# Optimization experiments

Hardware: AMD Instinct MI355X
Metric: run time of the kernel (lower is better)

## Reference

```python
import jax, jax.numpy as jnp
import numpy as np

N, E, IN, H, C, L = 50000, 800000, 256, 128, 50, 3
EPS = 1e-5  # BatchNorm1d eps


def setup_inputs() -> dict:
    key = jax.random.key(0)
    ks = jax.random.split(key, 16)
    s = 0.05  # weight init scale
    return dict(
        features=jax.random.normal(ks[0], (N, IN), jnp.float32),
        src=jax.random.randint(ks[1], (E,), 0, N, jnp.int32),
        dst=jax.random.randint(ks[2], (E,), 0, N, jnp.int32),
        w_in=jax.random.normal(ks[3], (IN, H), jnp.float32) * s,
        b_in=jnp.zeros((H,), jnp.float32),
        gc_w=jax.random.normal(ks[4], (L, H, H), jnp.float32) * s,
        gc_b=jnp.zeros((L, H), jnp.float32),
        bn_gamma=jnp.ones((L, H), jnp.float32),
        bn_beta=jnp.zeros((L, H), jnp.float32),
        bn_mean=jax.random.normal(ks[5], (L, H), jnp.float32) * 0.1,
        bn_var=jax.random.uniform(ks[6], (L, H), jnp.float32, 0.5, 1.5),
        attn_w1=jax.random.normal(ks[7], (2 * H, H), jnp.float32) * s,
        attn_b1=jnp.zeros((H,), jnp.float32),
        attn_w2=jax.random.normal(ks[8], (H, 1), jnp.float32) * s,
        attn_b2=jnp.zeros((1,), jnp.float32),
        agg_w=jax.random.normal(ks[9], (2 * H, H), jnp.float32) * s,
        agg_b=jnp.zeros((H,), jnp.float32),
        out_w=jax.random.normal(ks[10], (H, C), jnp.float32) * s,
        out_b=jnp.zeros((C,), jnp.float32),
    )


def reference(features, src, dst, w_in, b_in, gc_w, gc_b, bn_gamma, bn_beta,
              bn_mean, bn_var, attn_w1, attn_b1, attn_w2, attn_b2,
              agg_w, agg_b, out_w, out_b):
    seg = lambda v, i: jax.ops.segment_sum(v, i, num_segments=N)
    ones_e = jnp.ones((E,), features.dtype)
    in_deg = seg(ones_e, dst)    # [N] in-degree (dst side)
    out_deg = seg(ones_e, src)   # [N] out-degree (src side)

    # input_encoder (dropout = identity at inference)
    h = jax.nn.relu(features @ w_in + b_in)  # [N, H]

    # aggregate_neighbor_types: copy_u + mean (0 for zero in-degree)
    neigh = seg(h[src], dst) / jnp.maximum(in_deg, 1.0)[:, None]
    agg = jax.nn.relu(jnp.concatenate([h, neigh], axis=1) @ agg_w + agg_b)

    # relation attention: MLP -> sigmoid gate, gated residual add
    a = jax.nn.relu(jnp.concatenate([h, agg], axis=1) @ attn_w1 + attn_b1)
    attn = jax.nn.sigmoid(a @ attn_w2 + attn_b2)  # [N, 1]
    h_att = h + agg * attn

    # DGL GraphConv norm='both', clamp(min=1), aggregate-then-matmul
    inv_out = jnp.maximum(out_deg, 1.0)[:, None] ** -0.5
    inv_in = jnp.maximum(in_deg, 1.0)[:, None] ** -0.5
    for i in range(L):
        x = h_att if i == 0 else h
        rst = seg((x * inv_out)[src], dst) * inv_in  # normalized SpMM
        rst = rst @ gc_w[i] + gc_b[i]
        # BatchNorm1d (eval: running stats)
        rst = (rst - bn_mean[i]) * (bn_gamma[i] * jax.lax.rsqrt(bn_var[i] + EPS)) + bn_beta[i]
        rst = jax.nn.relu(rst)
        if i > 0:
            rst = rst + h  # residual
        h = rst

    return h @ out_w + out_b  # [N, C]
```

## Files before the change

### kernel.cpp

```cpp
#include <hip/hip_runtime.h>
#include <hip/hip_fp16.h>
#include <math.h>

constexpr int NN  = 50000;
constexpr int EE  = 800000;
constexpr int INF_ = 256;
constexpr int HF  = 128;
constexpr int CC  = 50;
constexpr long NH = (long)NN * HF;
constexpr int NSL = 32;
constexpr int ESL = EE / NSL;
constexpr int CHK = 12500;
#define EPSV 1e-5f

enum { EPI_RELU = 0, EPI_NONE = 1, EPI_BN = 2, EPI_BN_RES = 3, EPI_ATTN = 4 };
enum { H16_NONE = 0, H16_SCALED = 2 };

typedef __attribute__((ext_vector_type(4))) float f32x4;
typedef __attribute__((ext_vector_type(8))) _Float16 f16x8;


__global__ __launch_bounds__(256) void count_partial2_kernel(
    const int4* __restrict__ dst4, const int4* __restrict__ src4,
    unsigned* __restrict__ pd, unsigned* __restrict__ ps) {
  __shared__ unsigned cnt[CHK];
  int bb = blockIdx.x;
  const int which = bb >> 7;
  bb &= 127;
  const int4* keys4 = which ? src4 : dst4;
  unsigned* partials = which ? ps : pd;
  const int chunk = bb & 3;
  const int sl = bb >> 2;
  for (int i = threadIdx.x; i < CHK; i += 256) cnt[i] = 0;
  __syncthreads();
  const int base4 = sl * (ESL / 4);
  const int lo = chunk * CHK;
  for (int i = threadIdx.x; i < ESL / 4; i += 256) {
    int4 k = keys4[base4 + i];
    int a;
    a = k.x - lo; if ((unsigned)a < (unsigned)CHK) atomicAdd(&cnt[a], 1u);
    a = k.y - lo; if ((unsigned)a < (unsigned)CHK) atomicAdd(&cnt[a], 1u);
    a = k.z - lo; if ((unsigned)a < (unsigned)CHK) atomicAdd(&cnt[a], 1u);
    a = k.w - lo; if ((unsigned)a < (unsigned)CHK) atomicAdd(&cnt[a], 1u);
  }
  __syncthreads();
  unsigned* p = partials + (long)sl * NN + lo;
  for (int i = threadIdx.x; i < CHK; i += 256) p[i] = cnt[i];
}

__global__ __launch_bounds__(256) void deg_scan_kernel(
    const unsigned* __restrict__ pd, const unsigned* __restrict__ ps,
    int* __restrict__ row_ptr, int* __restrict__ bsum,
    float* __restrict__ inv_mean, float* __restrict__ inv_in,
    float* __restrict__ inv_out) {
  __shared__ int sh[256];
  int n = blockIdx.x * 256 + threadIdx.x;
  unsigned di = 0, dz = 0;
  if (n < NN) {
    #pragma unroll 8
    for (int sl = 0; sl < NSL; ++sl) {
      di += pd[(long)sl * NN + n];
      dz += ps[(long)sl * NN + n];
    }
    float fdi = fmaxf((float)di, 1.f), fdz = fmaxf((float)dz, 1.f);
    inv_mean[n] = 1.f / fdi;
    inv_in[n]  = rsqrtf(fdi);
    inv_out[n] = rsqrtf(fdz);
  }
  int v = (n < NN) ? (int)di : 0;
  sh[threadIdx.x] = v;
  __syncthreads();
  #pragma unroll
  for (int off = 1; off < 256; off <<= 1) {
    int tv = (threadIdx.x >= off) ? sh[threadIdx.x - off] : 0;
    __syncthreads();
    sh[threadIdx.x] += tv;
    __syncthreads();
  }
  if (n < NN) row_ptr[n] = sh[threadIdx.x] - v;
  if (threadIdx.x == 255) bsum[blockIdx.x] = sh[255];
}

__global__ __launch_bounds__(256) void scan_block_kernel(const int* __restrict__ counts,
                                                         int* excl, int* bsum, int n) {
  __shared__ int sh[256];
  int i = blockIdx.x * 256 + threadIdx.x;
  int v = (i < n) ? counts[i] : 0;
  sh[threadIdx.x] = v;
  __syncthreads();
  #pragma unroll
  for (int off = 1; off < 256; off <<= 1) {
    int tv = (threadIdx.x >= off) ? sh[threadIdx.x - off] : 0;
    __syncthreads();
    sh[threadIdx.x] += tv;
    __syncthreads();
  }
  if (i < n) excl[i] = sh[threadIdx.x] - v;
  if (threadIdx.x == 255 && bsum) bsum[blockIdx.x] = sh[255];
}

__global__ void cursor_init_kernel(const int* __restrict__ row_ptr, const int* __restrict__ bsum,
                                   const unsigned* __restrict__ pd,
                                   unsigned* __restrict__ cur0,
                                   const float* __restrict__ inv_mean,
                                   const float* __restrict__ inv_in,
                                   int4* __restrict__ nodeinfo) {
  int n = blockIdx.x * 256 + threadIdx.x;
  if (n >= NN) return;
  unsigned start = (unsigned)(row_ptr[n] + bsum[n >> 8]);
  unsigned run = start;
  #pragma unroll 8
  for (int sl = 0; sl < NSL; ++sl) {
    cur0[(long)sl * NN + n] = run;
    run += pd[(long)sl * NN + n];
  }
  nodeinfo[n] = make_int4((int)start, (int)run,
                          __float_as_int(inv_mean[n]), __float_as_int(inv_in[n]));
}

__global__ __launch_bounds__(256) void fill_partial_kernel(
    const int4* __restrict__ dst4, const int4* __restrict__ src4,
    const unsigned* __restrict__ cur0, int* __restrict__ col) {
  __shared__ unsigned cur[CHK];
  const int chunk = blockIdx.x & 3;
  const int sl = blockIdx.x >> 2;
  const int lo = chunk * CHK;
  const unsigned* c0 = cur0 + (long)sl * NN + lo;
  for (int i = threadIdx.x; i < CHK; i += 256) cur[i] = c0[i];
  __syncthreads();
  const int base4 = sl * (ESL / 4);
  for (int i = threadIdx.x; i < ESL / 4; i += 256) {
    int4 d = dst4[base4 + i];
    int4 s = src4[base4 + i];
    int a;
    a = d.x - lo; if ((unsigned)a < (unsigned)CHK) col[atomicAdd(&cur[a], 1u)] = s.x;
    a = d.y - lo; if ((unsigned)a < (unsigned)CHK) col[atomicAdd(&cur[a], 1u)] = s.y;
    a = d.z - lo; if ((unsigned)a < (unsigned)CHK) col[atomicAdd(&cur[a], 1u)] = s.z;
    a = d.w - lo; if ((unsigned)a < (unsigned)CHK) col[atomicAdd(&cur[a], 1u)] = s.w;
  }
}


__global__ __launch_bounds__(256) void spmm32p_kernel(
    const int4* __restrict__ nodeinfo, const int* __restrict__ cols,
    const __half* __restrict__ xs, int useW,
    __half* __restrict__ outh) {
  const int t = threadIdx.x;
  const int lane = t & 63;
  const int wv = t >> 6;
  const int b = blockIdx.x;
  const int xcd = b & 7;
  const int slice = xcd >> 1;
  const int sub = xcd & 1;
  const int npair = lane >> 5;
  const int node = (b >> 3) * 16 + sub * 8 + wv * 2 + npair;
  const int e8 = (lane >> 2) & 7;
  const int q4 = lane & 3;
  const __half* xb = xs + (long)slice * NN * 32 + q4 * 8;
  int4 ni = nodeinfo[node];
  const int e0 = ni.x, end = ni.y;
  const float d = __int_as_float(useW ? ni.w : ni.z);
  const int deg = end - e0;
  int dmax = deg > 0 ? deg : 0;
  {
    int od = __shfl_xor(dmax, 32, 64);
    dmax = dmax > od ? dmax : od;
  }
  const int kmax = (dmax + 7) >> 3;
  const int ecl = (end - 1) > 0 ? (end - 1) : 0;
  const __half2 z2 = __float2half2_rn(0.f);
  __half2 A0 = z2, A1 = z2, A2 = z2, A3 = z2;
  __half2 B0 = z2, B1 = z2, B2 = z2, B3 = z2;
  int k = 0;
  for (; k + 2 <= kmax; k += 2) {
    int ee0 = e0 + k * 8 + e8;
    int ee1 = ee0 + 8;
    bool m0 = ee0 < end, m1 = ee1 < end;
    int s0 = cols[m0 ? ee0 : ecl];
    int s1 = cols[m1 ? ee1 : ecl];
    f32x4 v0 = *(const f32x4*)(xb + (unsigned)s0 * 32u);
    f32x4 v1 = *(const f32x4*)(xb + (unsigned)s1 * 32u);
    const __half2* h0 = (const __half2*)&v0;
    const __half2* h1 = (const __half2*)&v1;
    A0 = __hadd2(A0, m0 ? h0[0] : z2); A1 = __hadd2(A1, m0 ? h0[1] : z2);
    A2 = __hadd2(A2, m0 ? h0[2] : z2); A3 = __hadd2(A3, m0 ? h0[3] : z2);
    B0 = __hadd2(B0, m1 ? h1[0] : z2); B1 = __hadd2(B1, m1 ? h1[1] : z2);
    B2 = __hadd2(B2, m1 ? h1[2] : z2); B3 = __hadd2(B3, m1 ? h1[3] : z2);
  }
  if (k < kmax) {
    int ee = e0 + k * 8 + e8;
    bool m = ee < end;
    int s = cols[m ? ee : ecl];
    f32x4 v = *(const f32x4*)(xb + (unsigned)s * 32u);
    const __half2* h = (const __half2*)&v;
    A0 = __hadd2(A0, m ? h[0] : z2); A1 = __hadd2(A1, m ? h[1] : z2);
    A2 = __hadd2(A2, m ? h[2] : z2); A3 = __hadd2(A3, m ? h[3] : z2);
  }
  A0 = __hadd2(A0, B0); A1 = __hadd2(A1, B1);
  A2 = __hadd2(A2, B2); A3 = __hadd2(A3, B3);
  float2 p0 = __half22float2(A0), p1 = __half22float2(A1);
  float2 p2 = __half22float2(A2), p3 = __half22float2(A3);
  float f0 = p0.x, f1 = p0.y, f2 = p1.x, f3 = p1.y;
  float f4 = p2.x, f5 = p2.y, f6 = p3.x, f7 = p3.y;
  {
    bool hi = (lane & 4) != 0;
    float t0 = hi ? f0 : f4, t1 = hi ? f1 : f5, t2 = hi ? f2 : f6, t3 = hi ? f3 : f7;
    t0 = __shfl_xor(t0, 4, 64); t1 = __shfl_xor(t1, 4, 64);
    t2 = __shfl_xor(t2, 4, 64); t3 = __shfl_xor(t3, 4, 64);
    f0 = (hi ? f4 : f0) + t0; f1 = (hi ? f5 : f1) + t1;
    f2 = (hi ? f6 : f2) + t2; f3 = (hi ? f7 : f3) + t3;
  }
  {
    bool hi = (lane & 8) != 0;
    float t0 = hi ? f0 : f2, t1 = hi ? f1 : f3;
    t0 = __shfl_xor(t0, 8, 64); t1 = __shfl_xor(t1, 8, 64);
    f0 = (hi ? f2 : f0) + t0; f1 = (hi ? f3 : f1) + t1;
  }
  float fin;
  {
    bool hi = (lane & 16) != 0;
    float t0 = hi ? f0 : f1;
    t0 = __shfl_xor(t0, 16, 64);
    fin = (hi ? f1 : f0) + t0;
  }
  int foff = q4 * 8 + ((lane >> 2) & 1) * 4 + ((lane >> 3) & 1) * 2 + ((lane >> 4) & 1);
  outh[((long)slice * NN + node) * 32 + foff] = __float2half(fin * d);
}


constexpr int SZ256 = 8 * 8 * 512;
constexpr int SZ128 = 4 * 8 * 512;
constexpr int SZOUT = 4 * 4 * 512;
constexpr int PK_TOTAL = 3 * SZ256 + 3 * SZ128 + SZOUT;

__global__ __launch_bounds__(256) void prepack_all_kernel(
    const float* __restrict__ w_in, const float* __restrict__ agg_w,
    const float* __restrict__ at1, const float* __restrict__ gc_w,
    const float* __restrict__ out_w, ushort* __restrict__ outbase) {
  int idx = blockIdx.x * 256 + threadIdx.x;
  if (idx >= PK_TOTAL) return;
  const float* W; int N, ldw, NTpad, local; ushort* outp;
  if (idx < 3 * SZ256) {
    int s = idx / SZ256; local = idx - s * SZ256;
    W = (s == 0) ? w_in : ((s == 1) ? agg_w : at1);
    N = HF; ldw = HF; NTpad = 8;
    outp = outbase + s * SZ256;
  } else if (idx < 3 * SZ256 + 3 * SZ128) {
    int r = idx - 3 * SZ256; int s = r / SZ128; local = r - s * SZ128;
    W = gc_w + (long)s * HF * HF; N = HF; ldw = HF; NTpad = 8;
    outp = outbase + 3 * SZ256 + s * SZ128;
  } else {
    local = idx - 3 * SZ256 - 3 * SZ128;
    W = out_w; N = CC; ldw = CC; NTpad = 4;
    outp = outbase + 3 * SZ256 + 3 * SZ128;
  }
  int j    = local & 7;
  int lane = (local >> 3) & 63;
  int rest = local >> 9;
  int nt = rest % NTpad;
  int kc = rest / NTpad;
  int k = kc * 32 + (lane >> 4) * 8 + j;
  int n = nt * 16 + (lane & 15);
  float w = (n < N) ? W[(long)k * ldw + n] : 0.f;
  outp[local] = __half_as_ushort(__float2half(w));
}


template<int KC, int NT, int NTP, int EPI, int H16, int ASRC, int OUTM, int COLSPLIT>
__global__ __launch_bounds__(256) void mgemm_kernel(
    const void* __restrict__ A1, int lda1,
    const void* __restrict__ A2,
    const ushort* __restrict__ Bf,
    const float* __restrict__ bias,
    const float* __restrict__ g, const float* __restrict__ be,
    const float* __restrict__ mu, const float* __restrict__ va,
    const __half* __restrict__ resp,
    float* __restrict__ outf, __half* __restrict__ outh, int ldc, int Ncols,
    __half* __restrict__ x16, const float* __restrict__ rowscale) {
  const int t = threadIdx.x;
  const int lane = t & 63;
  const int wid = t >> 6;
  const int rowbase = COLSPLIT ? (blockIdx.x * 32 + (wid >> 1) * 16)
                               : (blockIdx.x * 64 + wid * 16);
  const int colbase = COLSPLIT ? ((wid & 1) * NT * 16) : 0;
  const int arow = rowbase + (lane & 15);
  const int kgrp = (lane >> 4) * 8;
  const bool rowok = arow < NN;

  f32x4 acc[NT];
  #pragma unroll
  for (int n = 0; n < NT; ++n) acc[n] = (f32x4){0.f, 0.f, 0.f, 0.f};

  const f32x4 z4 = {0.f, 0.f, 0.f, 0.f};
  f32x4 fra[ASRC == 0 ? KC : 1], frb[ASRC == 0 ? KC : 1];
  uint4 areg[ASRC == 1 ? KC : 1];
  if (ASRC == 0) {
    #pragma unroll
    for (int kc = 0; kc < KC; ++kc) {
      const float* p = (const float*)A1 + (long)arow * lda1 + kc * 32 + kgrp;
      fra[kc] = rowok ? *(const f32x4*)p : z4;
      frb[kc] = rowok ? *(const f32x4*)(p + 4) : z4;
    }
  } else {
    #pragma unroll
    for (int kc = 0; kc < KC; ++kc) {
      const bool second = (KC == 8) && (kc >= 4);
      const ushort* At = (const ushort*)(second ? A2 : A1);
      int k0 = (second ? (kc - 4) : kc) * 32 + kgrp;
      const ushort* p = At + ((long)(k0 >> 5) * NN + arow) * 32 + (k0 & 31);
      areg[kc] = rowok ? *(const uint4*)p : make_uint4(0, 0, 0, 0);
    }
  }

  #pragma unroll
  for (int kc = 0; kc < KC; ++kc) {
    f16x8 av;
    if (ASRC == 0) {
      #pragma unroll
      for (int j = 0; j < 4; ++j) {
        av[j]     = (_Float16)fra[kc][j];
        av[j + 4] = (_Float16)frb[kc][j];
      }
    } else {
      union { uint4 u; f16x8 v; } cv;
      cv.u = areg[kc];
      av = cv.v;
    }
    const ushort* bp = Bf + ((long)kc * NTP * 64 + lane) * 8 + (long)colbase * 32;
    #pragma unroll
    for (int nt = 0; nt < NT; ++nt) {
      union { uint4 u; f16x8 v; } bv;
      bv.u = *(const uint4*)(bp + (long)nt * 512);
      acc[nt] = __builtin_amdgcn_mfma_f32_16x16x32_f16(av, bv.v, acc[nt], 0, 0, 0);
    }
  }

  const int colg = lane & 15;
  const int rsub = (lane >> 4) * 4;

  if (EPI == EPI_ATTN) {
    float part0 = 0.f, part1 = 0.f, part2 = 0.f, part3 = 0.f;
    #pragma unroll
    for (int nt = 0; nt < NT; ++nt) {
      int c = nt * 16 + colg;
      float w2v = g[c];
      float bb = bias[c];
      part0 = fmaf(fmaxf(acc[nt][0] + bb, 0.f), w2v, part0);
      part1 = fmaf(fmaxf(acc[nt][1] + bb, 0.f), w2v, part1);
      part2 = fmaf(fmaxf(acc[nt][2] + bb, 0.f), w2v, part2);
      part3 = fmaf(fmaxf(acc[nt][3] + bb, 0.f), w2v, part3);
    }
    #pragma unroll
    for (int m = 1; m <= 8; m <<= 1) {
      part0 += __shfl_xor(part0, m, 64);
      part1 += __shfl_xor(part1, m, 64);
      part2 += __shfl_xor(part2, m, 64);
      part3 += __shfl_xor(part3, m, 64);
    }
    const float b2v = be[0];
    float s0 = 1.f / (1.f + __expf(-(part0 + b2v)));
    float s1 = 1.f / (1.f + __expf(-(part1 + b2v)));
    float s2 = 1.f / (1.f + __expf(-(part2 + b2v)));
    float s3 = 1.f / (1.f + __expf(-(part3 + b2v)));
    const __half* h0t = (const __half*)A1;
    const __half* aggt = (const __half*)A2;
    #pragma unroll
    for (int nt = 0; nt < NT; ++nt) {
      int c = nt * 16 + colg;
      #pragma unroll
      for (int i = 0; i < 4; ++i) {
        int r = rowbase + rsub + i;
        if (r >= NN) continue;
        long sidx = ((long)(c >> 5) * NN + r) * 32 + (c & 31);
        float sv = (i == 0) ? s0 : ((i == 1) ? s1 : ((i == 2) ? s2 : s3));
        float h = __half2float(h0t[sidx]) + __half2float(aggt[sidx]) * sv;
        x16[sidx] = __float2half(h * rowscale[r]);
      }
    }
    return;
  }

  #pragma unroll
  for (int nt = 0; nt < NT; ++nt) {
    int c = colbase + nt * 16 + colg;
    if (c >= Ncols) continue;
    float bb = bias ? bias[c] : 0.f;
    float scale = 1.f, shift = 0.f;
    if (EPI == EPI_BN || EPI == EPI_BN_RES) {
      scale = g[c] * rsqrtf(va[c] + EPSV);
      shift = be[c] - mu[c] * scale;
    }
    #pragma unroll
    for (int i = 0; i < 4; ++i) {
      int r = rowbase + rsub + i;
      if (r >= NN) continue;
      long sidx = ((long)(c >> 5) * NN + r) * 32 + (c & 31);
      float v = acc[nt][i] + bb;
      if (EPI == EPI_RELU) {
        v = fmaxf(v, 0.f);
      } else if (EPI == EPI_BN || EPI == EPI_BN_RES) {
        v = fmaxf(v * scale + shift, 0.f);
        if (EPI == EPI_BN_RES) v += __half2float(resp[sidx]);
      }
      if (OUTM == 0) {
        outf[(long)r * ldc + c] = v;
      } else {
        outh[sidx] = __float2half(v);
        if (H16 == H16_SCALED) x16[sidx] = __float2half(v * rowscale[r]);
      }
    }
  }
}


extern "C" void kernel_launch(void* const* d_in, const int* in_sizes, int n_in,
                              void* d_out, int out_size, void* d_ws, size_t ws_size,
                              hipStream_t stream) {
  const float* features = (const float*)d_in[0];
  const int*   src      = (const int*)d_in[1];
  const int*   dst      = (const int*)d_in[2];
  const float* w_in     = (const float*)d_in[3];
  const float* b_in     = (const float*)d_in[4];
  const float* gc_w     = (const float*)d_in[5];
  const float* gc_b     = (const float*)d_in[6];
  const float* bn_gamma = (const float*)d_in[7];
  const float* bn_beta  = (const float*)d_in[8];
  const float* bn_mean  = (const float*)d_in[9];
  const float* bn_var   = (const float*)d_in[10];
  const float* attn_w1  = (const float*)d_in[11];
  const float* attn_b1  = (const float*)d_in[12];
  const float* attn_w2  = (const float*)d_in[13];
  const float* attn_b2  = (const float*)d_in[14];
  const float* agg_w    = (const float*)d_in[15];
  const float* agg_b    = (const float*)d_in[16];
  const float* out_w    = (const float*)d_in[17];
  const float* out_b    = (const float*)d_in[18];
  float* out = (float*)d_out;

  float* fbase = (float*)d_ws;
  float* inv_mean = fbase;
  float* inv_in   = inv_mean + NN;
  float* inv_out  = inv_in + NN;
  int* row_ptr = (int*)(inv_out + NN);
  int* bsum    = row_ptr + NN + 16;
  int* col     = bsum + 256;
  int4* nodeinfo = (int4*)(col + EE);

  ushort* pk = (ushort*)(nodeinfo + NN);
  ushort* win_f = pk;
  ushort* agg_f = pk + SZ256;
  ushort* at1_f = pk + 2 * SZ256;
  ushort* gcf0  = pk + 3 * SZ256;
  ushort* gcf1  = gcf0 + SZ128;
  ushort* gcf2  = gcf1 + SZ128;
  ushort* ow_f  = gcf2 + SZ128;

  __half* T0 = (__half*)(ow_f + SZOUT);
  __half* T1 = T0 + NH;
  __half* T2 = T1 + NH;
  __half* X16 = T2 + NH;

  unsigned* pd   = (unsigned*)T0;
  unsigned* ps   = pd + (long)NSL * NN;
  unsigned* cur0 = ps + (long)NSL * NN;

  dim3 b256(256);
  const int gN = (NN + 255) / 256;
  const int gblocks = (NN + 63) / 64;
  const int gsplit  = (NN + 31) / 32;
  const int gspmm = (NN / 16) * 8;
  const int gpre = NSL * 4;

  count_partial2_kernel<<<2 * gpre, b256, 0, stream>>>(
      (const int4*)dst, (const int4*)src, pd, ps);
  deg_scan_kernel<<<gN, b256, 0, stream>>>(pd, ps, row_ptr, bsum, inv_mean, inv_in, inv_out);
  scan_block_kernel<<<1, b256, 0, stream>>>(bsum, bsum, nullptr, gN);
  cursor_init_kernel<<<gN, b256, 0, stream>>>(row_ptr, bsum, pd, cur0, inv_mean, inv_in, nodeinfo);
  fill_partial_kernel<<<gpre, b256, 0, stream>>>((const int4*)dst, (const int4*)src, cur0, col);

  prepack_all_kernel<<<(PK_TOTAL + 255) / 256, b256, 0, stream>>>(
      w_in, agg_w, attn_w1, gc_w, out_w, pk);

  mgemm_kernel<8, 4, 8, EPI_RELU, H16_NONE, 0, 1, 1><<<gsplit, b256, 0, stream>>>(
      features, INF_, nullptr, win_f, b_in,
      nullptr, nullptr, nullptr, nullptr, nullptr,
      nullptr, T0, HF, HF, nullptr, nullptr);
  spmm32p_kernel<<<gspmm, b256, 0, stream>>>(nodeinfo, col, T0, 0, T1);
  mgemm_kernel<8, 4, 8, EPI_RELU, H16_NONE, 1, 1, 1><<<gsplit, b256, 0, stream>>>(
      T0, 0, T1, agg_f, agg_b,
      nullptr, nullptr, nullptr, nullptr, nullptr,
      nullptr, T2, HF, HF, nullptr, nullptr);
  mgemm_kernel<8, 8, 8, EPI_ATTN, H16_NONE, 1, 1, 0><<<gblocks, b256, 0, stream>>>(
      T0, 0, T2, at1_f, attn_b1,
      attn_w2, attn_b2, nullptr, nullptr, nullptr,
      nullptr, nullptr, HF, HF, X16, inv_out);

  spmm32p_kernel<<<gspmm, b256, 0, stream>>>(nodeinfo, col, X16, 1, T1);
  mgemm_kernel<4, 4, 8, EPI_BN, H16_SCALED, 1, 1, 1><<<gsplit, b256, 0, stream>>>(
      T1, 0, nullptr, gcf0, gc_b,
      bn_gamma, bn_beta, bn_mean, bn_var, nullptr,
      nullptr, T2, HF, HF, X16, inv_out);
  spmm32p_kernel<<<gspmm, b256, 0, stream>>>(nodeinfo, col, X16, 1, T1);
  mgemm_kernel<4, 4, 8, EPI_BN_RES, H16_SCALED, 1, 1, 1><<<gsplit, b256, 0, stream>>>(
      T1, 0, nullptr, gcf1, gc_b + HF,
      bn_gamma + HF, bn_beta + HF, bn_mean + HF, bn_var + HF, T2,
      nullptr, T0, HF, HF, X16, inv_out);
  spmm32p_kernel<<<gspmm, b256, 0, stream>>>(nodeinfo, col, X16, 1, T1);
  mgemm_kernel<4, 4, 8, EPI_BN_RES, H16_NONE, 1, 1, 1><<<gsplit, b256, 0, stream>>>(
      T1, 0, nullptr, gcf2, gc_b + 2 * HF,
      bn_gamma + 2 * HF, bn_beta + 2 * HF, bn_mean + 2 * HF, bn_var + 2 * HF, T0,
      nullptr, T2, HF, HF, nullptr, nullptr);

  mgemm_kernel<4, 4, 4, EPI_NONE, H16_NONE, 1, 0, 0><<<gblocks, b256, 0, stream>>>(
      T2, 0, nullptr, ow_f, out_b,
      nullptr, nullptr, nullptr, nullptr, nullptr,
      out, nullptr, CC, CC, nullptr, nullptr);
}
```

Measured before the change: 320.9 us.

## Reorder GraphConv to matmul-then-aggregate and fuse BN/ReLU/residual into SpMM

Each GraphConv layer now multiplies by the weight first, with the inv_out row scale applied in the GEMM epilogue, and then aggregates with the SpMM. This is valid because the scaled aggregation is linear and the weight is square (128x128). The bias, BatchNorm, ReLU and residual are folded into per-feature scale and shift vectors, computed once in the prepack kernel, and applied in the SpMM epilogue. This removes the separate scaled x16 copy written by each GEMM and the per-thread BN parameter computation, at the cost of reading the residual and BN vectors inside the SpMM. fp16 rounding now happens at different points, which may change numerics slightly.

```diff
diff --git a/kernel.cpp b/kernel.cpp
--- a/kernel.cpp
+++ b/kernel.cpp
@@ -13,8 +13,8 @@
 constexpr int CHK = 12500;
 #define EPSV 1e-5f
 
-enum { EPI_RELU = 0, EPI_NONE = 1, EPI_BN = 2, EPI_BN_RES = 3, EPI_ATTN = 4 };
-enum { H16_NONE = 0, H16_SCALED = 2 };
+enum { EPI_RELU = 0, EPI_NONE = 1, EPI_ATTN = 4 };
+enum { OUT_F32 = 0, OUT_F16 = 1, OUT_F16S = 2 };
 
 typedef __attribute__((ext_vector_type(4))) float f32x4;
 typedef __attribute__((ext_vector_type(8))) _Float16 f16x8;
@@ -141,9 +141,12 @@
 }
 
 
+template<int MODE>
 __global__ __launch_bounds__(256) void spmm32p_kernel(
     const int4* __restrict__ nodeinfo, const int* __restrict__ cols,
-    const __half* __restrict__ xs, int useW,
+    const __half* __restrict__ xs,
+    const float* __restrict__ bnsc, const float* __restrict__ bnsh,
+    const __half* __restrict__ resp,
     __half* __restrict__ outh) {
   const int t = threadIdx.x;
   const int lane = t & 63;
@@ -159,7 +162,7 @@
   const __half* xb = xs + (long)slice * NN * 32 + q4 * 8;
   int4 ni = nodeinfo[node];
   const int e0 = ni.x, end = ni.y;
-  const float d = __int_as_float(useW ? ni.w : ni.z);
+  const float d = __int_as_float(MODE == 0 ? ni.z : ni.w);
   const int deg = end - e0;
   int dmax = deg > 0 ? deg : 0;
   {
@@ -224,7 +227,14 @@
     fin = (hi ? f1 : f0) + t0;
   }
   int foff = q4 * 8 + ((lane >> 2) & 1) * 4 + ((lane >> 3) & 1) * 2 + ((lane >> 4) & 1);
-  outh[((long)slice * NN + node) * 32 + foff] = __float2half(fin * d);
+  long oidx = ((long)slice * NN + node) * 32 + foff;
+  float v = fin * d;
+  if (MODE >= 1) {
+    int f = slice * 32 + foff;
+    v = fmaxf(v * bnsc[f] + bnsh[f], 0.f);
+    if (MODE == 2) v += __half2float(resp[oidx]);
+  }
+  outh[oidx] = __float2half(v);
 }
 
 
@@ -232,13 +242,25 @@
 constexpr int SZ128 = 4 * 8 * 512;
 constexpr int SZOUT = 4 * 4 * 512;
 constexpr int PK_TOTAL = 3 * SZ256 + 3 * SZ128 + SZOUT;
+constexpr int PK_ALL = PK_TOTAL + 3 * HF;
 
 __global__ __launch_bounds__(256) void prepack_all_kernel(
     const float* __restrict__ w_in, const float* __restrict__ agg_w,
     const float* __restrict__ at1, const float* __restrict__ gc_w,
-    const float* __restrict__ out_w, ushort* __restrict__ outbase) {
+    const float* __restrict__ out_w, ushort* __restrict__ outbase,
+    const float* __restrict__ gc_b, const float* __restrict__ bn_gamma,
+    const float* __restrict__ bn_beta, const float* __restrict__ bn_mean,
+    const float* __restrict__ bn_var,
+    float* __restrict__ bnsc, float* __restrict__ bnsh) {
   int idx = blockIdx.x * 256 + threadIdx.x;
-  if (idx >= PK_TOTAL) return;
+  if (idx >= PK_ALL) return;
+  if (idx >= PK_TOTAL) {
+    int i = idx - PK_TOTAL;
+    float sc = bn_gamma[i] * rsqrtf(bn_var[i] + EPSV);
+    bnsc[i] = sc;
+    bnsh[i] = (gc_b[i] - bn_mean[i]) * sc + bn_beta[i];
+    return;
+  }
   const float* W; int N, ldw, NTpad, local; ushort* outp;
   if (idx < 3 * SZ256) {
     int s = idx / SZ256; local = idx - s * SZ256;
@@ -266,15 +288,13 @@
 }
 
 
-template<int KC, int NT, int NTP, int EPI, int H16, int ASRC, int OUTM, int COLSPLIT>
+template<int KC, int NT, int NTP, int EPI, int ASRC, int OUTM, int COLSPLIT>
 __global__ __launch_bounds__(256) void mgemm_kernel(
     const void* __restrict__ A1, int lda1,
     const void* __restrict__ A2,
     const ushort* __restrict__ Bf,
     const float* __restrict__ bias,
     const float* __restrict__ g, const float* __restrict__ be,
-    const float* __restrict__ mu, const float* __restrict__ va,
-    const __half* __restrict__ resp,
     float* __restrict__ outf, __half* __restrict__ outh, int ldc, int Ncols,
     __half* __restrict__ x16, const float* __restrict__ rowscale) {
   const int t = threadIdx.x;
@@ -374,7 +394,7 @@
         long sidx = ((long)(c >> 5) * NN + r) * 32 + (c & 31);
         float sv = (i == 0) ? s0 : ((i == 1) ? s1 : ((i == 2) ? s2 : s3));
         float h = __half2float(h0t[sidx]) + __half2float(aggt[sidx]) * sv;
-        x16[sidx] = __float2half(h * rowscale[r]);
+        x16[sidx] = __float2half(h);
       }
     }
     return;
@@ -385,28 +405,19 @@
     int c = colbase + nt * 16 + colg;
     if (c >= Ncols) continue;
     float bb = bias ? bias[c] : 0.f;
-    float scale = 1.f, shift = 0.f;
-    if (EPI == EPI_BN || EPI == EPI_BN_RES) {
-      scale = g[c] * rsqrtf(va[c] + EPSV);
-      shift = be[c] - mu[c] * scale;
-    }
     #pragma unroll
     for (int i = 0; i < 4; ++i) {
       int r = rowbase + rsub + i;
       if (r >= NN) continue;
       long sidx = ((long)(c >> 5) * NN + r) * 32 + (c & 31);
       float v = acc[nt][i] + bb;
-      if (EPI == EPI_RELU) {
-        v = fmaxf(v, 0.f);
-      } else if (EPI == EPI_BN || EPI == EPI_BN_RES) {
-        v = fmaxf(v * scale + shift, 0.f);
-        if (EPI == EPI_BN_RES) v += __half2float(resp[sidx]);
-      }
-      if (OUTM == 0) {
+      if (EPI == EPI_RELU) v = fmaxf(v, 0.f);
+      if (OUTM == OUT_F32) {
         outf[(long)r * ldc + c] = v;
+      } else if (OUTM == OUT_F16) {
+        outh[sidx] = __float2half(v);
       } else {
-        outh[sidx] = __float2half(v);
-        if (H16 == H16_SCALED) x16[sidx] = __float2half(v * rowscale[r]);
+        outh[sidx] = __float2half(v * rowscale[r]);
       }
     }
   }
@@ -454,8 +465,10 @@
   ushort* gcf1  = gcf0 + SZ128;
   ushort* gcf2  = gcf1 + SZ128;
   ushort* ow_f  = gcf2 + SZ128;
-
-  __half* T0 = (__half*)(ow_f + SZOUT);
+  float* bnsc = (float*)(ow_f + SZOUT);
+  float* bnsh = bnsc + 3 * HF;
+
+  __half* T0 = (__half*)(bnsh + 3 * HF);
   __half* T1 = T0 + NH;
   __half* T2 = T1 + NH;
   __half* X16 = T2 + NH;
@@ -478,41 +491,39 @@
   cursor_init_kernel<<<gN, b256, 0, stream>>>(row_ptr, bsum, pd, cur0, inv_mean, inv_in, nodeinfo);
   fill_partial_kernel<<<gpre, b256, 0, stream>>>((const int4*)dst, (const int4*)src, cur0, col);
 
-  prepack_all_kernel<<<(PK_TOTAL + 255) / 256, b256, 0, stream>>>(
-      w_in, agg_w, attn_w1, gc_w, out_w, pk);
-
-  mgemm_kernel<8, 4, 8, EPI_RELU, H16_NONE, 0, 1, 1><<<gsplit, b256, 0, stream>>>(
+  prepack_all_kernel<<<(PK_ALL + 255) / 256, b256, 0, stream>>>(
+      w_in, agg_w, attn_w1, gc_w, out_w, pk,
+      gc_b, bn_gamma, bn_beta, bn_mean, bn_var, bnsc, bnsh);
+
+  mgemm_kernel<8, 4, 8, EPI_RELU, 0, OUT_F16, 1><<<gsplit, b256, 0, stream>>>(
       features, INF_, nullptr, win_f, b_in,
-      nullptr, nullptr, nullptr, nullptr, nullptr,
-      nullptr, T0, HF, HF, nullptr, nullptr);
-  spmm32p_kernel<<<gspmm, b256, 0, stream>>>(nodeinfo, col, T0, 0, T1);
-  mgemm_kernel<8, 4, 8, EPI_RELU, H16_NONE, 1, 1, 1><<<gsplit, b256, 0, stream>>>(
+      nullptr, nullptr, nullptr, T0, HF, HF, nullptr, nullptr);
+  spmm32p_kernel<0><<<gspmm, b256, 0, stream>>>(
+      nodeinfo, col, T0, nullptr, nullptr, nullptr, T1);
+  mgemm_kernel<8, 4, 8, EPI_RELU, 1, OUT_F16, 1><<<gsplit, b256, 0, stream>>>(
       T0, 0, T1, agg_f, agg_b,
-      nullptr, nullptr, nullptr, nullptr, nullptr,
-      nullptr, T2, HF, HF, nullptr, nullptr);
-  mgemm_kernel<8, 8, 8, EPI_ATTN, H16_NONE, 1, 1, 0><<<gblocks, b256, 0, stream>>>(
+      nullptr, nullptr, nullptr, T2, HF, HF, nullptr, nullptr);
+  mgemm_kernel<8, 8, 8, EPI_ATTN, 1, OUT_F16, 0><<<gblocks, b256, 0, stream>>>(
       T0, 0, T2, at1_f, attn_b1,
-      attn_w2, attn_b2, nullptr, nullptr, nullptr,
-      nullptr, nullptr, HF, HF, X16, inv_out);
-
-  spmm32p_kernel<<<gspmm, b256, 0, stream>>>(nodeinfo, col, X16, 1, T1);
-  mgemm_kernel<4, 4, 8, EPI_BN, H16_SCALED, 1, 1, 1><<<gsplit, b256, 0, stream>>>(
-      T1, 0, nullptr, gcf0, gc_b,
-      bn_gamma, bn_beta, bn_mean, bn_var, nullptr,
-      nullptr, T2, HF, HF, X16, inv_out);
-  spmm32p_kernel<<<gspmm, b256, 0, stream>>>(nodeinfo, col, X16, 1, T1);
-  mgemm_kernel<4, 4, 8, EPI_BN_RES, H16_SCALED, 1, 1, 1><<<gsplit, b256, 0, stream>>>(
-      T1, 0, nullptr, gcf1, gc_b + HF,
-      bn_gamma + HF, bn_beta + HF, bn_mean + HF, bn_var + HF, T2,
-      nullptr, T0, HF, HF, X16, inv_out);
-  spmm32p_kernel<<<gspmm, b256, 0, stream>>>(nodeinfo, col, X16, 1, T1);
-  mgemm_kernel<4, 4, 8, EPI_BN_RES, H16_NONE, 1, 1, 1><<<gsplit, b256, 0, stream>>>(
-      T1, 0, nullptr, gcf2, gc_b + 2 * HF,
-      bn_gamma + 2 * HF, bn_beta + 2 * HF, bn_mean + 2 * HF, bn_var + 2 * HF, T0,
-      nullptr, T2, HF, HF, nullptr, nullptr);
-
-  mgemm_kernel<4, 4, 4, EPI_NONE, H16_NONE, 1, 0, 0><<<gblocks, b256, 0, stream>>>(
+      attn_w2, attn_b2, nullptr, nullptr, HF, HF, X16, nullptr);
+
+  mgemm_kernel<4, 4, 8, EPI_NONE, 1, OUT_F16S, 1><<<gsplit, b256, 0, stream>>>(
+      X16, 0, nullptr, gcf0, nullptr,
+      nullptr, nullptr, nullptr, T1, HF, HF, nullptr, inv_out);
+  spmm32p_kernel<1><<<gspmm, b256, 0, stream>>>(
+      nodeinfo, col, T1, bnsc, bnsh, nullptr, T2);
+  mgemm_kernel<4, 4, 8, EPI_NONE, 1, OUT_F16S, 1><<<gsplit, b256, 0, stream>>>(
+      T2, 0, nullptr, gcf1, nullptr,
+      nullptr, nullptr, nullptr, T1, HF, HF, nullptr, inv_out);
+  spmm32p_kernel<2><<<gspmm, b256, 0, stream>>>(
+      nodeinfo, col, T1, bnsc + HF, bnsh + HF, T2, X16);
+  mgemm_kernel<4, 4, 8, EPI_NONE, 1, OUT_F16S, 1><<<gsplit, b256, 0, stream>>>(
+      X16, 0, nullptr, gcf2, nullptr,
+      nullptr, nullptr, nullptr, T1, HF, HF, nullptr, inv_out);
+  spmm32p_kernel<2><<<gspmm, b256, 0, stream>>>(
+      nodeinfo, col, T1, bnsc + 2 * HF, bnsh + 2 * HF, X16, T2);
+
+  mgemm_kernel<4, 4, 4, EPI_NONE, 1, OUT_F32, 0><<<gblocks, b256, 0, stream>>>(
       T2, 0, nullptr, ow_f, out_b,
-      nullptr, nullptr, nullptr, nullptr, nullptr,
-      out, nullptr, CC, CC, nullptr, nullptr);
-}
+      nullptr, nullptr, out, nullptr, CC, CC, nullptr, nullptr);
+}
```

New measurement: 324.1 us. No clear change (+1.0%).
